# Kernel optimization log

Measured on AMD Instinct MI355X. Metric: run time of the kernel, lower is better.

The kernel has to match this reference:

```python
import jax, jax.numpy as jnp
import numpy as np

N_NODES = 100000
N_EDGES = 1600000
N_GRAPHS = 128


def setup_inputs() -> dict:
    key = jax.random.key(0)
    ks = jax.random.split(key, 8)
    x = jax.random.normal(ks[0], (N_NODES, 384), dtype=jnp.float32)
    edge_index = jax.random.randint(ks[1], (2, N_EDGES), 0, N_NODES, dtype=jnp.int64)
    batch = jnp.sort(jax.random.randint(ks[2], (N_NODES,), 0, N_GRAPHS, dtype=jnp.int64))
    W1 = jax.random.normal(ks[3], (384, 128), dtype=jnp.float32) * (1.0 / np.sqrt(384))
    b1 = jnp.zeros((128,), dtype=jnp.float32)
    W2 = jax.random.normal(ks[4], (128, 64), dtype=jnp.float32) * (1.0 / np.sqrt(128))
    b2 = jnp.zeros((64,), dtype=jnp.float32)
    Wlin = jax.random.normal(ks[5], (64, 2), dtype=jnp.float32) * (1.0 / np.sqrt(64))
    blin = jnp.zeros((2,), dtype=jnp.float32)
    return {"x": x, "edge_index": edge_index, "batch": batch,
            "W1": W1, "b1": b1, "W2": W2, "b2": b2, "Wlin": Wlin, "blin": blin}


def gcn_conv(x, src, dst, W, b, n_nodes):
    # PyG GCNConv: self-loops + symmetric normalization D^{-1/2} A_hat D^{-1/2},
    # linear transform first (out_dim < in_dim -> cheaper messages).
    h = x @ W  # [N, out]
    deg = jax.ops.segment_sum(jnp.ones_like(dst, dtype=h.dtype), dst,
                              num_segments=n_nodes) + 1.0  # self-loop weight
    dis = jax.lax.rsqrt(deg)  # deg >= 1 always (self-loop)
    norm = dis[src] * dis[dst]  # per-edge normalization [E]
    msg = h[src] * norm[:, None]  # gather + scale [E, out]
    agg = jax.ops.segment_sum(msg, dst, num_segments=n_nodes)
    agg = agg + h * (dis * dis)[:, None]  # self-loop contribution
    return agg + b


def reference(x, edge_index, batch, W1, b1, W2, b2, Wlin, blin):
    src, dst = edge_index[0], edge_index[1]
    n_nodes = x.shape[0]
    h = jax.nn.relu(gcn_conv(x, src, dst, W1, b1, n_nodes))
    h = jax.nn.relu(gcn_conv(h, src, dst, W2, b2, n_nodes))
    # global_mean_pool over graph ids
    sums = jax.ops.segment_sum(h, batch, num_segments=N_GRAPHS)
    cnts = jax.ops.segment_sum(jnp.ones((n_nodes,), dtype=h.dtype), batch,
                               num_segments=N_GRAPHS)
    pooled = sums / jnp.maximum(cnts, 1.0)[:, None]  # [G, 64]
    # dropout is identity in eval mode
    return pooled @ Wlin + blin  # [G, 2]
```

## Files before the change

### kernel.cpp

```cpp
#include <hip/hip_runtime.h>


#define NN 100000
#define NG 128
#define BNODES 256
#define NBUK ((NN + BNODES - 1) / BNODES)
#define BCAP 6144

typedef __attribute__((ext_vector_type(8))) short short8;
typedef __attribute__((ext_vector_type(8))) unsigned short u16x8;
typedef __attribute__((ext_vector_type(4))) float f32x4;

__device__ __forceinline__ unsigned short f2bf(float f) {
    union { float f; unsigned u; } v; v.f = f;
    unsigned r = v.u + 0x7fffu + ((v.u >> 16) & 1u);
    return (unsigned short)(r >> 16);
}
__device__ __forceinline__ float bf2f(unsigned short h) {
    union { unsigned u; float f; } v; v.u = ((unsigned)h) << 16;
    return v.f;
}

__global__ __launch_bounds__(256) void init_kernel(int* __restrict__ bcnt,
                                                   float* __restrict__ pooled,
                                                   float* __restrict__ cnt) {
    const int i = blockIdx.x * 256 + threadIdx.x;
    if (i < NBUK) bcnt[i] = 0;
    if (i < NG * 64) pooled[i] = 0.f;
    if (i < NG) cnt[i] = 0.f;
}

__global__ __launch_bounds__(256) void bucket_scatter(const int* __restrict__ src,
                                                      const int* __restrict__ dst,
                                                      int* __restrict__ bcnt,
                                                      int2* __restrict__ pairs, int E) {
    __shared__ int hist[NBUK];
    __shared__ int lbase[NBUK];
    __shared__ int lfill[NBUK];
    const int t = threadIdx.x;
    const int chunk = (E + gridDim.x - 1) / gridDim.x;
    const int lo = blockIdx.x * chunk;
    const int hi = min(E, lo + chunk);
    for (int b = t; b < NBUK; b += 256) { hist[b] = 0; lfill[b] = 0; }
    __syncthreads();
    for (int i = lo + t; i < hi; i += 256)
        atomicAdd(&hist[dst[i] >> 8], 1);
    __syncthreads();
    for (int b = t; b < NBUK; b += 256)
        lbase[b] = hist[b] ? atomicAdd(&bcnt[b], hist[b]) : 0;
    __syncthreads();
    for (int i = lo + t; i < hi; i += 256) {
        const int s = src[i], d = dst[i];
        const int b = d >> 8;
        const int off = atomicAdd(&lfill[b], 1);
        pairs[(size_t)b * BCAP + lbase[b] + off] = make_int2(s, d);
    }
}

__global__ __launch_bounds__(512) void bucket_scan(const int* __restrict__ bcnt,
                                                   int* __restrict__ bbase,
                                                   int* __restrict__ rowptr,
                                                   int N, int E) {
    __shared__ int sm[512];
    const int t = threadIdx.x;
    sm[t] = (t < NBUK) ? bcnt[t] : 0;
    __syncthreads();
    for (int d = 1; d < 512; d <<= 1) {
        int a = (t >= d) ? sm[t - d] : 0;
        __syncthreads();
        sm[t] += a;
        __syncthreads();
    }
    if (t <= NBUK) bbase[t] = (t == 0) ? 0 : sm[t - 1];
    if (t == 0) rowptr[N] = E;
}

__global__ __launch_bounds__(256) void bucket_build(const int2* __restrict__ pairs,
                                                    const int* __restrict__ bcnt,
                                                    const int* __restrict__ bbase,
                                                    int* __restrict__ rowptr,
                                                    float* __restrict__ dis,
                                                    int* __restrict__ col, int N) {
    __shared__ int cnt[BNODES];
    __shared__ int sm[BNODES];
    __shared__ int pref[BNODES];
    __shared__ int fillc[BNODES];
    const int b = blockIdx.x;
    const int t = threadIdx.x;
    const int nbase = b * BNODES;
    const int ecnt = bcnt[b];
    const int2* ep = pairs + (size_t)b * BCAP;
    const int gbase = bbase[b];

    cnt[t] = 0;
    fillc[t] = 0;
    __syncthreads();
    for (int i = t; i < ecnt; i += 256)
        atomicAdd(&cnt[ep[i].y & (BNODES - 1)], 1);
    __syncthreads();
    sm[t] = cnt[t];
    __syncthreads();
    for (int d = 1; d < 256; d <<= 1) {
        int a = (t >= d) ? sm[t - d] : 0;
        __syncthreads();
        sm[t] += a;
        __syncthreads();
    }
    pref[t] = sm[t] - cnt[t];
    const int node = nbase + t;
    if (node < N) {
        rowptr[node] = gbase + pref[t];
        dis[node] = rsqrtf((float)cnt[t] + 1.0f);
    }
    __syncthreads();
    for (int i = t; i < ecnt; i += 256) {
        const int2 e = ep[i];
        const int d = e.y & (BNODES - 1);
        const int pos = gbase + pref[d] + atomicAdd(&fillc[d], 1);
        col[pos] = e.x;
    }
}

__global__ __launch_bounds__(256) void pack_w(const float* __restrict__ W,
                                              unsigned short* __restrict__ packH,
                                              unsigned short* __restrict__ packL,
                                              int K, int BN) {
    const int idx = blockIdx.x * blockDim.x + threadIdx.x;
    if (idx >= K * BN) return;
    const int e = idx & 7;
    const int l = (idx >> 3) & 63;
    const int rest = idx >> 9;
    const int NF = BN >> 4;
    const int nf = rest % NF;
    const int ks = rest / NF;
    const int n = nf * 16 + (l & 15);
    const int k = ks * 32 + ((l >> 4) & 3) * 8 + e;
    const float v = W[(size_t)k * BN + n];
    const unsigned short h = f2bf(v);
    packH[idx] = h;
    packL[idx] = f2bf(v - bf2f(h));
}

template <int BN, int K>
__global__ __launch_bounds__(256) void gemm_mfma(const float* __restrict__ A,
                                                 const unsigned short* __restrict__ WpH,
                                                 const unsigned short* __restrict__ WpL,
                                                 const float* __restrict__ scale,
                                                 unsigned short* __restrict__ Out,
                                                 int N) {
    constexpr int BM = 64;
    constexpr int NK = K / 32;
    constexpr int WROWS = (BN == 128) ? 2 : 4;
    constexpr int WCOLS = (BN == 128) ? 2 : 1;
    constexpr int WTM = BM / WROWS;
    constexpr int MF = WTM / 16;
    constexpr int NFW = (BN / WCOLS) / 16;
    constexpr int NFB = BN / 16;

    __shared__ unsigned short AsH[2][BM / 16][512];

    const int t = threadIdx.x;
    const int wid = t >> 6, lane = t & 63;
    const int wr = wid / WCOLS, wc = wid % WCOLS;
    const int r0 = blockIdx.x * BM;

    const int s_row = t >> 2;
    const int s_kg = t & 3;
    const int s_lf = ((t >> 2) & 15) + s_kg * 16;
    const int s_m = s_row >> 4;

    const bool ok = (r0 + s_row) < N;
    const float* aptr = A + (size_t)(r0 + s_row) * K + s_kg * 8;

    auto loadA = [&](int ks, float4* v) {
        v[0] = v[1] = make_float4(0.f, 0.f, 0.f, 0.f);
        if (ok) {
            v[0] = *(const float4*)(aptr + ks * 32);
            v[1] = *(const float4*)(aptr + ks * 32 + 4);
        }
    };
    auto cvtwrite = [&](int buf, const float4* v) {
        short8 h;
        const float vv[8] = {v[0].x, v[0].y, v[0].z, v[0].w,
                             v[1].x, v[1].y, v[1].z, v[1].w};
#pragma unroll
        for (int j = 0; j < 8; ++j) h[j] = (short)f2bf(vv[j]);
        *(short8*)&AsH[buf][s_m][s_lf * 8] = h;
    };
    auto loadB = [&](int ks, short8* bH, short8* bL) {
#pragma unroll
        for (int n = 0; n < NFW; ++n) {
            const int nfg = wc * NFW + n;
            const int base = ((ks * NFB + nfg) * 64 + lane) * 8;
            bH[n] = *(const short8*)&WpH[base];
            bL[n] = *(const short8*)&WpL[base];
        }
    };

    f32x4 acc[MF][NFW];
#pragma unroll
    for (int m = 0; m < MF; ++m)
#pragma unroll
        for (int n = 0; n < NFW; ++n) acc[m][n] = (f32x4){0.f, 0.f, 0.f, 0.f};

    float4 av[2];
    loadA(0, av);
    cvtwrite(0, av);
    short8 bHc[NFW], bLc[NFW];
    loadB(0, bHc, bLc);

#pragma unroll
    for (int ks = 0; ks < NK; ++ks) {
        const int cur = ks & 1;
        __syncthreads();
        float4 avn[2];
        short8 bHn[NFW], bLn[NFW];
        if (ks + 1 < NK) {
            loadA(ks + 1, avn);
            loadB(ks + 1, bHn, bLn);
        }
#pragma unroll
        for (int m = 0; m < MF; ++m) {
            const int mf = wr * MF + m;
            const short8 aH = *(const short8*)&AsH[cur][mf][lane * 8];
#pragma unroll
            for (int n = 0; n < NFW; ++n) {
                acc[m][n] = __builtin_amdgcn_mfma_f32_16x16x32_bf16(aH, bHc[n], acc[m][n], 0, 0, 0);
                acc[m][n] = __builtin_amdgcn_mfma_f32_16x16x32_bf16(aH, bLc[n], acc[m][n], 0, 0, 0);
            }
        }
        if (ks + 1 < NK) {
            cvtwrite(cur ^ 1, avn);
#pragma unroll
            for (int n = 0; n < NFW; ++n) {
                bHc[n] = bHn[n];
                bLc[n] = bLn[n];
            }
        }
    }

#pragma unroll
    for (int m = 0; m < MF; ++m) {
        const int row0 = r0 + wr * WTM + m * 16 + ((lane >> 4) << 2);
        float sc[4];
#pragma unroll
        for (int r = 0; r < 4; ++r) sc[r] = (row0 + r < N) ? scale[row0 + r] : 0.f;
#pragma unroll
        for (int n = 0; n < NFW; ++n) {
            const int cn = wc * (NFW * 16) + n * 16 + (lane & 15);
#pragma unroll
            for (int r = 0; r < 4; ++r) {
                if (row0 + r < N)
                    Out[(size_t)(row0 + r) * BN + cn] = f2bf(acc[m][n][r] * sc[r]);
            }
        }
    }
}

template <int COLS>
__global__ __launch_bounds__(256) void agg_gather(const int* __restrict__ rowptr,
                                                  const int* __restrict__ col,
                                                  const float* __restrict__ dis,
                                                  const unsigned short* __restrict__ Hs,
                                                  const float* __restrict__ bias,
                                                  float* __restrict__ Out, int N) {
    constexpr int NPW = (COLS == 128) ? 1 : 2;
    constexpr int LPN = 64 / NPW;
    constexpr int LPR = COLS / 8;
    constexpr int NSG = LPN / LPR;
    const int gw = (int)((blockIdx.x * blockDim.x + threadIdx.x) >> 6);
    const int lane = threadIdx.x & 63;
    const int sub = lane / LPN;
    const int nl = lane % LPN;
    const int esub = nl / LPR;
    const int sl = nl % LPR;
    const int node = gw * NPW + sub;
    const int lgbase = sub * LPN;

    float acc[8];
#pragma unroll
    for (int k = 0; k < 8; ++k) acc[k] = 0.f;

    int base = 0, len = 0;
    const int nodec = (node < N) ? node : 0;
    if (node < N) {
        base = rowptr[node];
        len = rowptr[node + 1] - base;
    }

    for (int j0 = 0; j0 < len; j0 += LPN) {
        const int remain = min(LPN, len - j0);
        const int sidx = (nl < remain) ? col[base + j0 + nl] : nodec;
        const int qtr = (remain + NSG - 1) / NSG;
        const int off = esub * qtr;
        int u = 0;
        for (; u + 8 <= qtr; u += 8) {
            u16x8 hv[8];
            float wv[8];
#pragma unroll
            for (int b = 0; b < 8; ++b) {
                const int idx = off + u + b;
                const int s = __shfl(sidx, lgbase + idx);
                wv[b] = (idx < remain) ? 1.f : 0.f;
                hv[b] = *(const u16x8*)(Hs + (size_t)s * COLS + sl * 8);
            }
#pragma unroll
            for (int b = 0; b < 8; ++b)
#pragma unroll
                for (int k = 0; k < 8; ++k)
                    acc[k] = fmaf(bf2f(hv[b][k]), wv[b], acc[k]);
        }
        for (; u + 4 <= qtr; u += 4) {
            u16x8 hv[4];
            float wv[4];
#pragma unroll
            for (int b = 0; b < 4; ++b) {
                const int idx = off + u + b;
                const int s = __shfl(sidx, lgbase + idx);
                wv[b] = (idx < remain) ? 1.f : 0.f;
                hv[b] = *(const u16x8*)(Hs + (size_t)s * COLS + sl * 8);
            }
#pragma unroll
            for (int b = 0; b < 4; ++b)
#pragma unroll
                for (int k = 0; k < 8; ++k)
                    acc[k] = fmaf(bf2f(hv[b][k]), wv[b], acc[k]);
        }
        for (; u < qtr; ++u) {
            const int idx = off + u;
            const int s = __shfl(sidx, lgbase + idx);
            const float w = (idx < remain) ? 1.f : 0.f;
            const u16x8 hv = *(const u16x8*)(Hs + (size_t)s * COLS + sl * 8);
#pragma unroll
            for (int k = 0; k < 8; ++k)
                acc[k] = fmaf(bf2f(hv[k]), w, acc[k]);
        }
    }

#pragma unroll
    for (int k = 0; k < 8; ++k) {
        acc[k] += __shfl_xor(acc[k], LPR);
        acc[k] += __shfl_xor(acc[k], 2 * LPR);
    }

    if (node < N && esub == 0) {
        const float dd = dis[node];
        const u16x8 hsb = *(const u16x8*)(Hs + (size_t)node * COLS + sl * 8);
        const f32x4 bv0 = *(const f32x4*)(bias + sl * 8);
        const f32x4 bv1 = *(const f32x4*)(bias + sl * 8 + 4);
        f32x4 o0, o1;
#pragma unroll
        for (int k = 0; k < 4; ++k) {
            o0[k] = fmaxf(fmaf(acc[k] + bf2f(hsb[k]), dd, bv0[k]), 0.f);
            o1[k] = fmaxf(fmaf(acc[k + 4] + bf2f(hsb[k + 4]), dd, bv1[k]), 0.f);
        }
        *(f32x4*)(Out + (size_t)node * COLS + sl * 8) = o0;
        *(f32x4*)(Out + (size_t)node * COLS + sl * 8 + 4) = o1;
    }
}

__global__ __launch_bounds__(256) void pool_kernel(const float* __restrict__ H,
                                                   const int* __restrict__ batch,
                                                   float* __restrict__ pooled,
                                                   float* __restrict__ cnt, int N) {
    const int c = threadIdx.x & 63;
    const int w = threadIdx.x >> 6;
    const int row0 = blockIdx.x * 128 + w * 32;
    if (row0 >= N) return;
    const int nr = min(32, N - row0);

    float v[32];
    int b[32];
#pragma unroll
    for (int i = 0; i < 32; ++i) {
        const int r = row0 + i;
        if (i < nr) {
            v[i] = H[(size_t)r * 64 + c];
            b[i] = batch[r];
        } else {
            v[i] = 0.f;
            b[i] = -1;
        }
    }
    int cur = b[0];
    float sum = 0.f, csum = 0.f;
#pragma unroll
    for (int i = 0; i < 32; ++i) {
        if (i < nr) {
            if (b[i] != cur) {
                atomicAdd(&pooled[cur * 64 + c], sum);
                if (c == 0) atomicAdd(&cnt[cur], csum);
                cur = b[i];
                sum = 0.f;
                csum = 0.f;
            }
            sum += v[i];
            csum += 1.f;
        }
    }
    atomicAdd(&pooled[cur * 64 + c], sum);
    if (c == 0) atomicAdd(&cnt[cur], csum);
}

__global__ __launch_bounds__(256) void final_kernel(const float* __restrict__ pooled,
                                                    const float* __restrict__ cnt,
                                                    const float* __restrict__ Wlin,
                                                    const float* __restrict__ blin,
                                                    float* __restrict__ out) {
    const int t = threadIdx.x;
    const int g = t >> 1, o = t & 1;
    const float inv = 1.0f / fmaxf(cnt[g], 1.0f);
    float s = 0.f;
#pragma unroll
    for (int j = 0; j < 64; ++j) s = fmaf(pooled[g * 64 + j], Wlin[j * 2 + o], s);
    out[t] = s * inv + blin[o];
}

extern "C" void kernel_launch(void* const* d_in, const int* in_sizes, int n_in,
                              void* d_out, int out_size, void* d_ws, size_t ws_size,
                              hipStream_t stream) {
    const float* x     = (const float*)d_in[0];
    const int*   edge  = (const int*)d_in[1];
    const int*   batch = (const int*)d_in[2];
    const float* W1    = (const float*)d_in[3];
    const float* b1    = (const float*)d_in[4];
    const float* W2    = (const float*)d_in[5];
    const float* b2    = (const float*)d_in[6];
    const float* Wlin  = (const float*)d_in[7];
    const float* blin  = (const float*)d_in[8];
    float* out = (float*)d_out;

    const int N = NN;
    const int E = in_sizes[1] / 2;
    const int* src = edge;
    const int* dst = edge + E;

    char* ws = (char*)d_ws;
    size_t off = 0;
    auto alloc = [&](size_t bytes) -> void* {
        void* p = ws + off;
        off += (bytes + 511) & ~(size_t)511;
        return p;
    };
    float* dis    = (float*)alloc((size_t)N * 4);
    int*   rowptr = (int*)alloc((size_t)(N + 1) * 4);
    int*   bcnt   = (int*)alloc((size_t)NBUK * 4);
    int*   bbase  = (int*)alloc((size_t)(NBUK + 1) * 4);
    int*   col    = (int*)alloc((size_t)E * 4);
    int2*  pairs  = (int2*)alloc((size_t)NBUK * BCAP * 8);
    unsigned short* w1h = (unsigned short*)alloc((size_t)384 * 128 * 2);
    unsigned short* w1l = (unsigned short*)alloc((size_t)384 * 128 * 2);
    unsigned short* w2h = (unsigned short*)alloc((size_t)128 * 64 * 2);
    unsigned short* w2l = (unsigned short*)alloc((size_t)128 * 64 * 2);
    unsigned short* h1bf = (unsigned short*)alloc((size_t)N * 128 * 2);
    float* agg1   = (float*)alloc((size_t)N * 128 * 4);
    float* pooled = (float*)alloc((size_t)NG * 64 * 4);
    float* cnt    = (float*)alloc((size_t)NG * 4);
    unsigned short* h2bf = h1bf;
    float* agg2 = agg1;

    init_kernel<<<(NG * 64 + 255) / 256, 256, 0, stream>>>(bcnt, pooled, cnt);

    pack_w<<<(384 * 128 + 255) / 256, 256, 0, stream>>>(W1, w1h, w1l, 384, 128);
    pack_w<<<(128 * 64 + 255) / 256, 256, 0, stream>>>(W2, w2h, w2l, 128, 64);

    bucket_scatter<<<512, 256, 0, stream>>>(src, dst, bcnt, pairs, E);
    bucket_scan<<<1, 512, 0, stream>>>(bcnt, bbase, rowptr, N, E);
    bucket_build<<<NBUK, 256, 0, stream>>>(pairs, bcnt, bbase, rowptr, dis, col, N);

    const int gblocks = (N + 63) / 64;
    gemm_mfma<128, 384><<<gblocks, 256, 0, stream>>>(x, w1h, w1l, dis, h1bf, N);
    agg_gather<128><<<(N + 3) / 4, 256, 0, stream>>>(rowptr, col, dis, h1bf, b1, agg1, N);

    gemm_mfma<64, 128><<<gblocks, 256, 0, stream>>>(agg1, w2h, w2l, dis, h2bf, N);
    agg_gather<64><<<(N + 7) / 8, 256, 0, stream>>>(rowptr, col, dis, h2bf, b2, agg2, N);

    pool_kernel<<<(N + 127) / 128, 256, 0, stream>>>(agg2, batch, pooled, cnt, N);
    final_kernel<<<1, 256, 0, stream>>>(pooled, cnt, Wlin, blin, out);
}
```

Measured before the change: 256.4 us.

## Stage GEMM A tiles via direct global-to-LDS loads, convert to bf16 after LDS

Replaces the register round-trip for the fp32 A operand (global load, bf16 convert, LDS write) with global_load_lds DMA that writes fp32 straight into shared memory. The bf16 conversion moves to the consumer side when fragments are read from LDS. This aims to cut VGPR pressure and the issue slots spent on staging. In exchange, LDS footprint doubles, the same rows may be converted more than once, and there is no explicit wait on the async LDS writes before the barrier.

```diff
diff --git a/kernel.cpp b/kernel.cpp
--- a/kernel.cpp
+++ b/kernel.cpp
@@ -19,6 +19,12 @@
 __device__ __forceinline__ float bf2f(unsigned short h) {
     union { unsigned u; float f; } v; v.u = ((unsigned)h) << 16;
     return v.f;
+}
+
+__device__ __forceinline__ void gload_lds16(const float* g, void* l) {
+    __builtin_amdgcn_global_load_lds(
+        (const __attribute__((address_space(1))) void*)g,
+        (__attribute__((address_space(3))) void*)l, 16, 0, 0);
 }
 
 __global__ __launch_bounds__(256) void init_kernel(int* __restrict__ bcnt,
@@ -157,35 +163,21 @@
     constexpr int NFW = (BN / WCOLS) / 16;
     constexpr int NFB = BN / 16;
 
-    __shared__ unsigned short AsH[2][BM / 16][512];
+    __shared__ float AsF[2][4][16][32];
 
     const int t = threadIdx.x;
     const int wid = t >> 6, lane = t & 63;
     const int wr = wid / WCOLS, wc = wid % WCOLS;
     const int r0 = blockIdx.x * BM;
 
-    const int s_row = t >> 2;
-    const int s_kg = t & 3;
-    const int s_lf = ((t >> 2) & 15) + s_kg * 16;
-    const int s_m = s_row >> 4;
-
-    const bool ok = (r0 + s_row) < N;
-    const float* aptr = A + (size_t)(r0 + s_row) * K + s_kg * 8;
-
-    auto loadA = [&](int ks, float4* v) {
-        v[0] = v[1] = make_float4(0.f, 0.f, 0.f, 0.f);
-        if (ok) {
-            v[0] = *(const float4*)(aptr + ks * 32);
-            v[1] = *(const float4*)(aptr + ks * 32 + 4);
-        }
-    };
-    auto cvtwrite = [&](int buf, const float4* v) {
-        short8 h;
-        const float vv[8] = {v[0].x, v[0].y, v[0].z, v[0].w,
-                             v[1].x, v[1].y, v[1].z, v[1].w};
-#pragma unroll
-        for (int j = 0; j < 8; ++j) h[j] = (short)f2bf(vv[j]);
-        *(short8*)&AsH[buf][s_m][s_lf * 8] = h;
+    const int dmarow0 = min(r0 + wid * 16 + (lane >> 3), NN - 1);
+    const int dmarow1 = min(r0 + wid * 16 + 8 + (lane >> 3), NN - 1);
+    const float* dmap0 = A + (size_t)dmarow0 * K + (lane & 7) * 4;
+    const float* dmap1 = A + (size_t)dmarow1 * K + (lane & 7) * 4;
+
+    auto stageA = [&](int buf, int ks) {
+        gload_lds16(dmap0 + ks * 32, &AsF[buf][wid][0][0]);
+        gload_lds16(dmap1 + ks * 32, &AsF[buf][wid][8][0]);
     };
     auto loadB = [&](int ks, short8* bH, short8* bL) {
 #pragma unroll
@@ -203,9 +195,7 @@
 #pragma unroll
         for (int n = 0; n < NFW; ++n) acc[m][n] = (f32x4){0.f, 0.f, 0.f, 0.f};
 
-    float4 av[2];
-    loadA(0, av);
-    cvtwrite(0, av);
+    stageA(0, 0);
     short8 bHc[NFW], bLc[NFW];
     loadB(0, bHc, bLc);
 
@@ -213,16 +203,26 @@
     for (int ks = 0; ks < NK; ++ks) {
         const int cur = ks & 1;
         __syncthreads();
-        float4 avn[2];
         short8 bHn[NFW], bLn[NFW];
         if (ks + 1 < NK) {
-            loadA(ks + 1, avn);
+            stageA(cur ^ 1, ks + 1);
             loadB(ks + 1, bHn, bLn);
         }
 #pragma unroll
         for (int m = 0; m < MF; ++m) {
             const int mf = wr * MF + m;
-            const short8 aH = *(const short8*)&AsH[cur][mf][lane * 8];
+            const float* fp = &AsF[cur][mf][lane & 15][(lane >> 4) * 8];
+            const f32x4 f0 = *(const f32x4*)fp;
+            const f32x4 f1 = *(const f32x4*)(fp + 4);
+            short8 aH;
+            aH[0] = (short)f2bf(f0[0]);
+            aH[1] = (short)f2bf(f0[1]);
+            aH[2] = (short)f2bf(f0[2]);
+            aH[3] = (short)f2bf(f0[3]);
+            aH[4] = (short)f2bf(f1[0]);
+            aH[5] = (short)f2bf(f1[1]);
+            aH[6] = (short)f2bf(f1[2]);
+            aH[7] = (short)f2bf(f1[3]);
 #pragma unroll
             for (int n = 0; n < NFW; ++n) {
                 acc[m][n] = __builtin_amdgcn_mfma_f32_16x16x32_bf16(aH, bHc[n], acc[m][n], 0, 0, 0);
@@ -230,7 +230,6 @@
             }
         }
         if (ks + 1 < NK) {
-            cvtwrite(cur ^ 1, avn);
 #pragma unroll
             for (int n = 0; n < NFW; ++n) {
                 bHc[n] = bHn[n];
```

Result: faster. 249.7 us (-2.6%).
